# Optimization experiments

Hardware: AMD Instinct MI355X
Metric: run time of the kernel (lower is better)

Reference implementation:

```python
import jax, jax.numpy as jnp
import numpy as np

BN_EPS = 1e-5


def mesh_conv(x, gemm, W):
    # x: [B, C, E], gemm: [B, E, 4] neighbor edge indices, W: [O, C, 5]
    # gather the 4 neighbor edge features per edge (per batch element)
    nbr = jax.vmap(lambda xb, gb: xb[:, gb])(x, gemm)  # [B, C, E, 4]
    f1, f2, f3, f4 = nbr[..., 0], nbr[..., 1], nbr[..., 2], nbr[..., 3]
    # MeshCNN symmetric functions over opposite neighbors
    f = jnp.stack(
        [x, f1 + f3, f2 + f4, jnp.abs(f1 - f3), jnp.abs(f2 - f4)], axis=-1
    )  # [B, C, E, 5]
    # Conv2d(in, out, kernel=(1,5), bias=False) == contraction over (C, 5)
    return jnp.einsum('bcek,ock->boe', f, W)  # [B, O, E]


def batchnorm_relu(x, gamma, beta):
    # BatchNorm2d in training mode (stats over batch and edge dims), applied
    # to relu(x) as in the original: bn(F.relu(x)); x is [B, C, E]
    h = jax.nn.relu(x)
    mean = jnp.mean(h, axis=(0, 2), keepdims=True)
    var = jnp.var(h, axis=(0, 2), keepdims=True)
    h = (h - mean) * jax.lax.rsqrt(var + BN_EPS)
    return h * gamma[None, :, None] + beta[None, :, None]


def setup_inputs() -> dict:
    key = jax.random.key(0)
    ks = jax.random.split(key, 5)
    B, C_in, C_out, E = 4, 128, 256, 30000
    x = jax.random.normal(ks[0], (B, C_in, E), dtype=jnp.float32)
    gemm = jax.random.randint(ks[1], (B, E, 4), 0, E, dtype=jnp.int32)
    W0 = jax.random.normal(ks[2], (C_out, C_in, 5), dtype=jnp.float32) * (1.0 / np.sqrt(C_in * 5))
    gamma1 = jnp.ones((C_out,), dtype=jnp.float32)
    beta1 = jnp.zeros((C_out,), dtype=jnp.float32)
    W1 = jax.random.normal(ks[3], (C_out, C_out, 5), dtype=jnp.float32) * (1.0 / np.sqrt(C_out * 5))
    return {"x": x, "gemm": gemm, "W0": W0, "gamma1": gamma1, "beta1": beta1, "W1": W1}


def reference(x, gemm, W0, gamma1, beta1, W1):
    x = mesh_conv(x, gemm, W0)          # conv0
    x1 = x                               # residual branch
    x = batchnorm_relu(x, gamma1, beta1)  # bn1(relu(x))
    x = mesh_conv(x, gemm, W1)          # conv1
    x = x + x1                           # residual add
    return jax.nn.relu(x)                # [B, C_out, E]
```

## Files before the change

kernel.cpp:

```cpp
#include <hip/hip_runtime.h>
#include <stdint.h>


#define BB 4
#define CIN 128
#define COUT 256
#define EE 30000
#define BN 64
#define NTILES 469
#define BC 64
#define KCH 320
#define PITCH 328
#define NBLK (NTILES * BB)

typedef __attribute__((ext_vector_type(8))) short bf16x8;
typedef __attribute__((ext_vector_type(4))) float f32x4;

static __device__ __forceinline__ unsigned f2bf1(float f) {
    union { float f; unsigned u; } v; v.f = f;
    return (v.u + 0x7fffu + ((v.u >> 16) & 1u)) >> 16;
}
static __device__ __forceinline__ unsigned pack2(float lo, float hi) {
    return f2bf1(lo) | (f2bf1(hi) << 16);
}
static __device__ __forceinline__ float bf2f(unsigned h) {
    union { unsigned u; float f; } v; v.u = h << 16;
    return v.f;
}

union RowU { int4 i4[2]; unsigned u[8]; };
union F16U { float4 f4[4]; float f[16]; };

__global__ __launch_bounds__(256) void k_transpose(const float* __restrict__ x,
                                                   unsigned short* __restrict__ xT) {
    __shared__ float tile[64][CIN + 1];
    const int t = threadIdx.x;
    const int e0 = blockIdx.x * 64;
    const int b = blockIdx.y;
    const int el = t & 63;
    const bool ok = (e0 + el) < EE;
    const float* xb = x + (size_t)b * CIN * EE;
#pragma unroll
    for (int cc = 0; cc < CIN / 4; ++cc) {
        const int c = cc * 4 + (t >> 6);
        tile[el][c] = ok ? xb[(size_t)c * EE + e0 + el] : 0.f;
    }
    __syncthreads();
    const int el2 = t >> 2, cq = t & 3;
    if (e0 + el2 < EE) {
        unsigned ov[16];
#pragma unroll
        for (int i = 0; i < 16; ++i)
            ov[i] = pack2(tile[el2][cq * 32 + 2 * i], tile[el2][cq * 32 + 2 * i + 1]);
        int4* dst = (int4*)(xT + ((size_t)b * EE + e0 + el2) * CIN + cq * 32);
#pragma unroll
        for (int j = 0; j < 4; ++j)
            dst[j] = make_int4((int)ov[4 * j], (int)ov[4 * j + 1], (int)ov[4 * j + 2], (int)ov[4 * j + 3]);
    }
}

__global__ __launch_bounds__(256) void k_wprep(const float* __restrict__ W,
                                               unsigned short* __restrict__ Wf,
                                               int C, int K) {
    const int id = blockIdx.x * 256 + threadIdx.x;
    if (id >= 256 * K) return;
    const int m = id / K;
    const int G = id % K;
    const int chunk = G / KCH;
    const int r = G % KCH;
    const int k = r / BC;
    const int c = chunk * BC + (r % BC);
    const float val = W[((size_t)m * C + c) * 5 + k];
    Wf[((size_t)(G / 32) * 256 + m) * 32 + (G % 32)] = (unsigned short)f2bf1(val);
}

__global__ __launch_bounds__(256) void k_stats(const float* __restrict__ partials,
                                               const float* __restrict__ gamma,
                                               const float* __restrict__ beta,
                                               float* __restrict__ ss) {
    const int ch = blockIdx.x;
    const int t = threadIdx.x;
    float s = 0.f, q = 0.f;
    for (int i = t; i < NBLK; i += 256) {
        s += partials[(size_t)i * 512 + ch];
        q += partials[(size_t)i * 512 + 256 + ch];
    }
    __shared__ float ls[256], lq[256];
    ls[t] = s; lq[t] = q;
    __syncthreads();
    for (int off = 128; off > 0; off >>= 1) {
        if (t < off) { ls[t] += ls[t + off]; lq[t] += lq[t + off]; }
        __syncthreads();
    }
    if (t == 0) {
        const float inv = 1.f / (float)(BB * EE);
        const float mean = ls[0] * inv;
        const float var = lq[0] * inv - mean * mean;
        const float sc = gamma[ch] * rsqrtf(var + 1e-5f);
        ss[ch] = sc;
        ss[COUT + ch] = beta[ch] - mean * sc;
    }
}

template <int C, int CHUNKS, int IS1>
__global__ __launch_bounds__(256) void k_conv(
    const unsigned short* __restrict__ xin,
    const int* __restrict__ gmm,
    const unsigned short* __restrict__ Wf,
    const float* __restrict__ ss,
    unsigned short* __restrict__ x1,
    unsigned short* __restrict__ rT,
    float* __restrict__ partials,
    float* __restrict__ out) {
    __shared__ unsigned short f_lds[64 * PITCH];
    const int t = threadIdx.x;
    const int w = t >> 6, lane = t & 63;
    const int ml = lane & 15, g = lane >> 4;
    const int tile = blockIdx.x, b = blockIdx.y;
    const int e0 = tile * BN;

    const int be = t >> 2, bq = t & 3;
    const int eb = e0 + be;
    const int ec = (eb < EE) ? eb : 0;
    const int4 nb = *(const int4*)(gmm + ((size_t)b * EE + ec) * 4);

    const unsigned short* xb = xin + (size_t)b * EE * C;
    const unsigned short* rowc = xb + (size_t)ec * C;
    const unsigned short* row1 = xb + (size_t)nb.x * C;
    const unsigned short* row2 = xb + (size_t)nb.y * C;
    const unsigned short* row3 = xb + (size_t)nb.z * C;
    const unsigned short* row4 = xb + (size_t)nb.w * C;

    f32x4 acc[4][4];
#pragma unroll
    for (int i = 0; i < 4; ++i)
#pragma unroll
        for (int j = 0; j < 4; ++j)
            acc[i][j] = (f32x4){0.f, 0.f, 0.f, 0.f};

#pragma unroll 1
    for (int chunk = 0; chunk < CHUNKS; ++chunk) {
        const int cb = chunk * BC + bq * 16;

        F16U sc, sh;
        if (IS1) {
#pragma unroll
            for (int q = 0; q < 4; ++q) {
                sc.f4[q] = *(const float4*)(ss + cb + 4 * q);
                sh.f4[q] = *(const float4*)(ss + COUT + cb + 4 * q);
            }
        }

        unsigned o0[8], o1[8], o2[8], o3[8], o4[8];
        {
            RowU va, vb;
            va.i4[0] = *(const int4*)(row1 + cb); va.i4[1] = *(const int4*)(row1 + cb + 8);
            vb.i4[0] = *(const int4*)(row3 + cb); vb.i4[1] = *(const int4*)(row3 + cb + 8);
#pragma unroll
            for (int j = 0; j < 8; ++j) {
                float a0 = bf2f(va.u[j] & 0xffffu), a1 = bf2f(va.u[j] >> 16);
                float b0 = bf2f(vb.u[j] & 0xffffu), b1 = bf2f(vb.u[j] >> 16);
                if (IS1) {
                    a0 = fmaf(a0, sc.f[2 * j], sh.f[2 * j]); a1 = fmaf(a1, sc.f[2 * j + 1], sh.f[2 * j + 1]);
                    b0 = fmaf(b0, sc.f[2 * j], sh.f[2 * j]); b1 = fmaf(b1, sc.f[2 * j + 1], sh.f[2 * j + 1]);
                }
                o1[j] = pack2(a0 + b0, a1 + b1);
                o3[j] = pack2(fabsf(a0 - b0), fabsf(a1 - b1));
            }
        }
        {
            RowU va, vb;
            va.i4[0] = *(const int4*)(row2 + cb); va.i4[1] = *(const int4*)(row2 + cb + 8);
            vb.i4[0] = *(const int4*)(row4 + cb); vb.i4[1] = *(const int4*)(row4 + cb + 8);
#pragma unroll
            for (int j = 0; j < 8; ++j) {
                float a0 = bf2f(va.u[j] & 0xffffu), a1 = bf2f(va.u[j] >> 16);
                float b0 = bf2f(vb.u[j] & 0xffffu), b1 = bf2f(vb.u[j] >> 16);
                if (IS1) {
                    a0 = fmaf(a0, sc.f[2 * j], sh.f[2 * j]); a1 = fmaf(a1, sc.f[2 * j + 1], sh.f[2 * j + 1]);
                    b0 = fmaf(b0, sc.f[2 * j], sh.f[2 * j]); b1 = fmaf(b1, sc.f[2 * j + 1], sh.f[2 * j + 1]);
                }
                o2[j] = pack2(a0 + b0, a1 + b1);
                o4[j] = pack2(fabsf(a0 - b0), fabsf(a1 - b1));
            }
        }
        {
            RowU v;
            v.i4[0] = *(const int4*)(rowc + cb); v.i4[1] = *(const int4*)(rowc + cb + 8);
#pragma unroll
            for (int j = 0; j < 8; ++j) {
                float c0 = bf2f(v.u[j] & 0xffffu), c1 = bf2f(v.u[j] >> 16);
                if (IS1) {
                    c0 = fmaf(c0, sc.f[2 * j], sh.f[2 * j]); c1 = fmaf(c1, sc.f[2 * j + 1], sh.f[2 * j + 1]);
                }
                o0[j] = pack2(c0, c1);
            }
        }

        __syncthreads();
        {
            unsigned short* bp = &f_lds[be * PITCH + bq * 16];
            *(int4*)(bp + 0 * BC)     = make_int4((int)o0[0], (int)o0[1], (int)o0[2], (int)o0[3]);
            *(int4*)(bp + 0 * BC + 8) = make_int4((int)o0[4], (int)o0[5], (int)o0[6], (int)o0[7]);
            *(int4*)(bp + 1 * BC)     = make_int4((int)o1[0], (int)o1[1], (int)o1[2], (int)o1[3]);
            *(int4*)(bp + 1 * BC + 8) = make_int4((int)o1[4], (int)o1[5], (int)o1[6], (int)o1[7]);
            *(int4*)(bp + 2 * BC)     = make_int4((int)o2[0], (int)o2[1], (int)o2[2], (int)o2[3]);
            *(int4*)(bp + 2 * BC + 8) = make_int4((int)o2[4], (int)o2[5], (int)o2[6], (int)o2[7]);
            *(int4*)(bp + 3 * BC)     = make_int4((int)o3[0], (int)o3[1], (int)o3[2], (int)o3[3]);
            *(int4*)(bp + 3 * BC + 8) = make_int4((int)o3[4], (int)o3[5], (int)o3[6], (int)o3[7]);
            *(int4*)(bp + 4 * BC)     = make_int4((int)o4[0], (int)o4[1], (int)o4[2], (int)o4[3]);
            *(int4*)(bp + 4 * BC + 8) = make_int4((int)o4[4], (int)o4[5], (int)o4[6], (int)o4[7]);
        }
        __syncthreads();

        const unsigned short* wp = Wf + (size_t)chunk * (KCH / 32) * COUT * 32;
#pragma unroll 2
        for (int kk = 0; kk < KCH / 32; ++kk) {
            union { int4 i; bf16x8 h; } af[4], bfr[4];
#pragma unroll
            for (int fm = 0; fm < 4; ++fm)
                af[fm].i = *(const int4*)(wp + ((size_t)kk * COUT + (w * 64 + fm * 16 + ml)) * 32 + g * 8);
#pragma unroll
            for (int fn = 0; fn < 4; ++fn)
                bfr[fn].i = *(const int4*)&f_lds[(fn * 16 + ml) * PITCH + kk * 32 + g * 8];
#pragma unroll
            for (int fm = 0; fm < 4; ++fm)
#pragma unroll
                for (int fn = 0; fn < 4; ++fn)
                    acc[fm][fn] = __builtin_amdgcn_mfma_f32_16x16x32_bf16(af[fm].h, bfr[fn].h, acc[fm][fn], 0, 0, 0);
        }
    }

    const size_t fragbase = (((size_t)b * NTILES + tile) * 4 + w) * 16;
    if (!IS1) {
#pragma unroll
        for (int fm = 0; fm < 4; ++fm) {
#pragma unroll
            for (int fn = 0; fn < 4; ++fn) {
                const int fi = fm * 4 + fn;
                uint2 pk;
                pk.x = pack2(acc[fm][fn][0], acc[fm][fn][1]);
                pk.y = pack2(acc[fm][fn][2], acc[fm][fn][3]);
                *(uint2*)(x1 + (fragbase + fi) * 256 + lane * 4) = pk;
                const int e = e0 + fn * 16 + ml;
                if (e < EE) {
                    uint2 pr;
                    pr.x = pack2(fmaxf(acc[fm][fn][0], 0.f), fmaxf(acc[fm][fn][1], 0.f));
                    pr.y = pack2(fmaxf(acc[fm][fn][2], 0.f), fmaxf(acc[fm][fn][3], 0.f));
                    *(uint2*)(rT + ((size_t)b * EE + e) * COUT + w * 64 + fm * 16 + g * 4) = pr;
                }
            }
        }
        float ks = 0.f, kq = 0.f;
#pragma unroll
        for (int fm = 0; fm < 4; ++fm) {
#pragma unroll
            for (int r = 0; r < 4; ++r) {
                float s = 0.f, q2 = 0.f;
#pragma unroll
                for (int fn = 0; fn < 4; ++fn) {
                    const int e = e0 + fn * 16 + ml;
                    const float v = (e < EE) ? fmaxf(acc[fm][fn][r], 0.f) : 0.f;
                    s += v; q2 += v * v;
                }
                s += __shfl_xor(s, 1); s += __shfl_xor(s, 2);
                s += __shfl_xor(s, 4); s += __shfl_xor(s, 8);
                q2 += __shfl_xor(q2, 1); q2 += __shfl_xor(q2, 2);
                q2 += __shfl_xor(q2, 4); q2 += __shfl_xor(q2, 8);
                if (ml == fm * 4 + r) { ks = s; kq = q2; }
            }
        }
        const int ch = w * 64 + (ml >> 2) * 16 + g * 4 + (ml & 3);
        float* pp = partials + ((size_t)b * NTILES + tile) * 512;
        pp[ch] = ks;
        pp[256 + ch] = kq;
    } else {
#pragma unroll
        for (int fm = 0; fm < 4; ++fm) {
#pragma unroll
            for (int fn = 0; fn < 4; ++fn) {
                const int fi = fm * 4 + fn;
                const uint2 pk = *(const uint2*)(x1 + (fragbase + fi) * 256 + lane * 4);
                const int e = e0 + fn * 16 + ml;
                if (e < EE) {
                    const int chb = w * 64 + fm * 16 + g * 4;
                    float* op = out + ((size_t)b * COUT + chb) * EE + e;
                    op[0]              = fmaxf(acc[fm][fn][0] + bf2f(pk.x & 0xffffu), 0.f);
                    op[(size_t)EE]     = fmaxf(acc[fm][fn][1] + bf2f(pk.x >> 16), 0.f);
                    op[(size_t)2 * EE] = fmaxf(acc[fm][fn][2] + bf2f(pk.y & 0xffffu), 0.f);
                    op[(size_t)3 * EE] = fmaxf(acc[fm][fn][3] + bf2f(pk.y >> 16), 0.f);
                }
            }
        }
    }
}

extern "C" void kernel_launch(void* const* d_in, const int* in_sizes, int n_in,
                              void* d_out, int out_size, void* d_ws, size_t ws_size,
                              hipStream_t stream) {
    const float* x = (const float*)d_in[0];
    const int* gmm = (const int*)d_in[1];
    const float* W0 = (const float*)d_in[2];
    const float* gamma = (const float*)d_in[3];
    const float* beta = (const float*)d_in[4];
    const float* W1 = (const float*)d_in[5];
    float* out = (float*)d_out;

    char* ws = (char*)d_ws;
    unsigned short* xT  = (unsigned short*)(ws);
    unsigned short* Wf0 = (unsigned short*)(ws + 30720000);
    unsigned short* Wf1 = (unsigned short*)(ws + 31047680);
    unsigned short* x1  = (unsigned short*)(ws + 31703040);
    unsigned short* rT  = (unsigned short*)(ws + 93175808);
    float* partials     = (float*)(ws + 154615808);
    float* ss           = (float*)(ws + 158457856);

    k_transpose<<<dim3(NTILES, BB), 256, 0, stream>>>(x, xT);
    k_wprep<<<dim3(640), 256, 0, stream>>>(W0, Wf0, CIN, 640);
    k_wprep<<<dim3(1280), 256, 0, stream>>>(W1, Wf1, COUT, 1280);
    k_conv<CIN, 2, 0><<<dim3(NTILES, BB), 256, 0, stream>>>(
        xT, gmm, Wf0, nullptr, x1, rT, partials, nullptr);
    k_stats<<<dim3(256), 256, 0, stream>>>(partials, gamma, beta, ss);
    k_conv<COUT, 4, 1><<<dim3(NTILES, BB), 256, 0, stream>>>(
        rT, gmm, Wf1, ss, x1, nullptr, nullptr, out);
}
```

Measured before the change: 530.5 us.

## Fold BN affine into conv1 weights and bias, prefetch gathers, remap grid

Moves the batchnorm scale into the second conv's weights (using abs(scale) for the abs-difference terms) and the shift into a per-output bias computed by a new kernel. This removes the per-element FMA normalisation from the gather stage. Also adds register double-buffering of the neighbour-row loads, a 1D grid that interleaves batches, launch_bounds for 2 blocks per CU, intrinsic bf16 packing, and a cheaper partial-stats reduction. The fold is exact only for gamma-scaled rows, and applying abs(scale) to the weights assumes the shift cancels inside the difference terms. Double buffering raises register pressure.

```diff
diff --git a/kernel.cpp b/kernel.cpp
--- a/kernel.cpp
+++ b/kernel.cpp
@@ -1,4 +1,5 @@
 #include <hip/hip_runtime.h>
+#include <hip/hip_bf16.h>
 #include <stdint.h>
 
 
@@ -12,24 +13,25 @@
 #define KCH 320
 #define PITCH 328
 #define NBLK (NTILES * BB)
+#define GRID1 1880
 
 typedef __attribute__((ext_vector_type(8))) short bf16x8;
 typedef __attribute__((ext_vector_type(4))) float f32x4;
 
-static __device__ __forceinline__ unsigned f2bf1(float f) {
-    union { float f; unsigned u; } v; v.f = f;
-    return (v.u + 0x7fffu + ((v.u >> 16) & 1u)) >> 16;
-}
-static __device__ __forceinline__ unsigned pack2(float lo, float hi) {
-    return f2bf1(lo) | (f2bf1(hi) << 16);
-}
-static __device__ __forceinline__ float bf2f(unsigned h) {
-    union { unsigned u; float f; } v; v.u = h << 16;
-    return v.f;
-}
-
-union RowU { int4 i4[2]; unsigned u[8]; };
-union F16U { float4 f4[4]; float f[16]; };
+static __device__ __forceinline__ float blo(unsigned u) {
+    union { unsigned u; float f; } v; v.u = u << 16; return v.f;
+}
+static __device__ __forceinline__ float bhi(unsigned u) {
+    union { unsigned u; float f; } v; v.u = u & 0xffff0000u; return v.f;
+}
+static __device__ __forceinline__ unsigned pk2(float lo, float hi) {
+    __hip_bfloat162 h = __float22bfloat162_rn(float2{lo, hi});
+    union { __hip_bfloat162 h; unsigned u; } v; v.h = h; return v.u;
+}
+static __device__ __forceinline__ unsigned short bf1(float f) {
+    __hip_bfloat16 h = __float2bfloat16(f);
+    union { __hip_bfloat16 h; unsigned short u; } v; v.h = h; return v.u;
+}
 
 __global__ __launch_bounds__(256) void k_transpose(const float* __restrict__ x,
                                                    unsigned short* __restrict__ xT) {
@@ -51,7 +53,7 @@
         unsigned ov[16];
 #pragma unroll
         for (int i = 0; i < 16; ++i)
-            ov[i] = pack2(tile[el2][cq * 32 + 2 * i], tile[el2][cq * 32 + 2 * i + 1]);
+            ov[i] = pk2(tile[el2][cq * 32 + 2 * i], tile[el2][cq * 32 + 2 * i + 1]);
         int4* dst = (int4*)(xT + ((size_t)b * EE + e0 + el2) * CIN + cq * 32);
 #pragma unroll
         for (int j = 0; j < 4; ++j)
@@ -61,6 +63,7 @@
 
 __global__ __launch_bounds__(256) void k_wprep(const float* __restrict__ W,
                                                unsigned short* __restrict__ Wf,
+                                               const float* __restrict__ ss,
                                                int C, int K) {
     const int id = blockIdx.x * 256 + threadIdx.x;
     if (id >= 256 * K) return;
@@ -70,8 +73,12 @@
     const int r = G % KCH;
     const int k = r / BC;
     const int c = chunk * BC + (r % BC);
-    const float val = W[((size_t)m * C + c) * 5 + k];
-    Wf[((size_t)(G / 32) * 256 + m) * 32 + (G % 32)] = (unsigned short)f2bf1(val);
+    float val = W[((size_t)m * C + c) * 5 + k];
+    if (ss) {
+        const float sc = ss[c];
+        val *= (k < 3) ? sc : fabsf(sc);
+    }
+    Wf[((size_t)(G / 32) * 256 + m) * 32 + (G % 32)] = bf1(val);
 }
 
 __global__ __launch_bounds__(256) void k_stats(const float* __restrict__ partials,
@@ -102,12 +109,29 @@
     }
 }
 
+__global__ __launch_bounds__(256) void k_bias(const float* __restrict__ W1,
+                                              const float* __restrict__ ss,
+                                              float* __restrict__ bias) {
+    const int o = blockIdx.x, t = threadIdx.x;
+    const float sh = ss[COUT + t];
+    const float* wr = W1 + ((size_t)o * COUT + t) * 5;
+    float v = sh * (wr[0] + 2.f * (wr[1] + wr[2]));
+    __shared__ float red[256];
+    red[t] = v;
+    __syncthreads();
+    for (int off = 128; off > 0; off >>= 1) {
+        if (t < off) red[t] += red[t + off];
+        __syncthreads();
+    }
+    if (t == 0) bias[o] = red[0];
+}
+
 template <int C, int CHUNKS, int IS1>
-__global__ __launch_bounds__(256) void k_conv(
+__global__ __launch_bounds__(256, 2) void k_conv(
     const unsigned short* __restrict__ xin,
     const int* __restrict__ gmm,
     const unsigned short* __restrict__ Wf,
-    const float* __restrict__ ss,
+    const float* __restrict__ bias,
     unsigned short* __restrict__ x1,
     unsigned short* __restrict__ rT,
     float* __restrict__ partials,
@@ -116,7 +140,10 @@
     const int t = threadIdx.x;
     const int w = t >> 6, lane = t & 63;
     const int ml = lane & 15, g = lane >> 4;
-    const int tile = blockIdx.x, b = blockIdx.y;
+    const int i = blockIdx.x;
+    const int b = (i & 7) >> 1;
+    const int tile = ((i >> 3) << 1) | (i & 1);
+    if (tile >= NTILES) return;
     const int e0 = tile * BN;
 
     const int be = t >> 2, bq = t & 3;
@@ -133,75 +160,51 @@
 
     f32x4 acc[4][4];
 #pragma unroll
-    for (int i = 0; i < 4; ++i)
-#pragma unroll
-        for (int j = 0; j < 4; ++j)
-            acc[i][j] = (f32x4){0.f, 0.f, 0.f, 0.f};
-
-#pragma unroll 1
-    for (int chunk = 0; chunk < CHUNKS; ++chunk) {
+    for (int ii = 0; ii < 4; ++ii)
+#pragma unroll
+        for (int jj = 0; jj < 4; ++jj)
+            acc[ii][jj] = (f32x4){0.f, 0.f, 0.f, 0.f};
+
+    int4 bufA[10], bufB[10];
+
+    auto stage = [&](int chunk, int4* dst) {
         const int cb = chunk * BC + bq * 16;
-
-        F16U sc, sh;
-        if (IS1) {
-#pragma unroll
-            for (int q = 0; q < 4; ++q) {
-                sc.f4[q] = *(const float4*)(ss + cb + 4 * q);
-                sh.f4[q] = *(const float4*)(ss + COUT + cb + 4 * q);
-            }
-        }
-
-        unsigned o0[8], o1[8], o2[8], o3[8], o4[8];
-        {
-            RowU va, vb;
-            va.i4[0] = *(const int4*)(row1 + cb); va.i4[1] = *(const int4*)(row1 + cb + 8);
-            vb.i4[0] = *(const int4*)(row3 + cb); vb.i4[1] = *(const int4*)(row3 + cb + 8);
-#pragma unroll
-            for (int j = 0; j < 8; ++j) {
-                float a0 = bf2f(va.u[j] & 0xffffu), a1 = bf2f(va.u[j] >> 16);
-                float b0 = bf2f(vb.u[j] & 0xffffu), b1 = bf2f(vb.u[j] >> 16);
-                if (IS1) {
-                    a0 = fmaf(a0, sc.f[2 * j], sh.f[2 * j]); a1 = fmaf(a1, sc.f[2 * j + 1], sh.f[2 * j + 1]);
-                    b0 = fmaf(b0, sc.f[2 * j], sh.f[2 * j]); b1 = fmaf(b1, sc.f[2 * j + 1], sh.f[2 * j + 1]);
-                }
-                o1[j] = pack2(a0 + b0, a1 + b1);
-                o3[j] = pack2(fabsf(a0 - b0), fabsf(a1 - b1));
-            }
-        }
-        {
-            RowU va, vb;
-            va.i4[0] = *(const int4*)(row2 + cb); va.i4[1] = *(const int4*)(row2 + cb + 8);
-            vb.i4[0] = *(const int4*)(row4 + cb); vb.i4[1] = *(const int4*)(row4 + cb + 8);
-#pragma unroll
-            for (int j = 0; j < 8; ++j) {
-                float a0 = bf2f(va.u[j] & 0xffffu), a1 = bf2f(va.u[j] >> 16);
-                float b0 = bf2f(vb.u[j] & 0xffffu), b1 = bf2f(vb.u[j] >> 16);
-                if (IS1) {
-                    a0 = fmaf(a0, sc.f[2 * j], sh.f[2 * j]); a1 = fmaf(a1, sc.f[2 * j + 1], sh.f[2 * j + 1]);
-                    b0 = fmaf(b0, sc.f[2 * j], sh.f[2 * j]); b1 = fmaf(b1, sc.f[2 * j + 1], sh.f[2 * j + 1]);
-                }
-                o2[j] = pack2(a0 + b0, a1 + b1);
-                o4[j] = pack2(fabsf(a0 - b0), fabsf(a1 - b1));
-            }
-        }
-        {
-            RowU v;
-            v.i4[0] = *(const int4*)(rowc + cb); v.i4[1] = *(const int4*)(rowc + cb + 8);
-#pragma unroll
-            for (int j = 0; j < 8; ++j) {
-                float c0 = bf2f(v.u[j] & 0xffffu), c1 = bf2f(v.u[j] >> 16);
-                if (IS1) {
-                    c0 = fmaf(c0, sc.f[2 * j], sh.f[2 * j]); c1 = fmaf(c1, sc.f[2 * j + 1], sh.f[2 * j + 1]);
-                }
-                o0[j] = pack2(c0, c1);
-            }
+        dst[0] = *(const int4*)(row1 + cb); dst[1] = *(const int4*)(row1 + cb + 8);
+        dst[2] = *(const int4*)(row3 + cb); dst[3] = *(const int4*)(row3 + cb + 8);
+        dst[4] = *(const int4*)(row2 + cb); dst[5] = *(const int4*)(row2 + cb + 8);
+        dst[6] = *(const int4*)(row4 + cb); dst[7] = *(const int4*)(row4 + cb + 8);
+        dst[8] = *(const int4*)(rowc + cb); dst[9] = *(const int4*)(rowc + cb + 8);
+    };
+
+    auto step = [&](int chunk, const int4* cur, int4* nxt, bool donext) {
+        if (donext) stage(chunk + 1, nxt);
+
+        const unsigned* u13a = (const unsigned*)&cur[0];
+        const unsigned* u13b = (const unsigned*)&cur[2];
+        const unsigned* u24a = (const unsigned*)&cur[4];
+        const unsigned* u24b = (const unsigned*)&cur[6];
+        const unsigned* uc   = (const unsigned*)&cur[8];
+        unsigned o1[8], o2[8], o3[8], o4[8];
+#pragma unroll
+        for (int j = 0; j < 8; ++j) {
+            const float a0 = blo(u13a[j]), a1 = bhi(u13a[j]);
+            const float b0 = blo(u13b[j]), b1 = bhi(u13b[j]);
+            o1[j] = pk2(a0 + b0, a1 + b1);
+            o3[j] = pk2(fabsf(a0 - b0), fabsf(a1 - b1));
+        }
+#pragma unroll
+        for (int j = 0; j < 8; ++j) {
+            const float a0 = blo(u24a[j]), a1 = bhi(u24a[j]);
+            const float b0 = blo(u24b[j]), b1 = bhi(u24b[j]);
+            o2[j] = pk2(a0 + b0, a1 + b1);
+            o4[j] = pk2(fabsf(a0 - b0), fabsf(a1 - b1));
         }
 
         __syncthreads();
         {
             unsigned short* bp = &f_lds[be * PITCH + bq * 16];
-            *(int4*)(bp + 0 * BC)     = make_int4((int)o0[0], (int)o0[1], (int)o0[2], (int)o0[3]);
-            *(int4*)(bp + 0 * BC + 8) = make_int4((int)o0[4], (int)o0[5], (int)o0[6], (int)o0[7]);
+            *(int4*)(bp + 0 * BC)     = make_int4((int)uc[0], (int)uc[1], (int)uc[2], (int)uc[3]);
+            *(int4*)(bp + 0 * BC + 8) = make_int4((int)uc[4], (int)uc[5], (int)uc[6], (int)uc[7]);
             *(int4*)(bp + 1 * BC)     = make_int4((int)o1[0], (int)o1[1], (int)o1[2], (int)o1[3]);
             *(int4*)(bp + 1 * BC + 8) = make_int4((int)o1[4], (int)o1[5], (int)o1[6], (int)o1[7]);
             *(int4*)(bp + 2 * BC)     = make_int4((int)o2[0], (int)o2[1], (int)o2[2], (int)o2[3]);
@@ -229,66 +232,84 @@
                 for (int fn = 0; fn < 4; ++fn)
                     acc[fm][fn] = __builtin_amdgcn_mfma_f32_16x16x32_bf16(af[fm].h, bfr[fn].h, acc[fm][fn], 0, 0, 0);
         }
+    };
+
+    stage(0, bufA);
+#pragma unroll 1
+    for (int cp = 0; cp < CHUNKS / 2; ++cp) {
+        step(2 * cp, bufA, bufB, true);
+        step(2 * cp + 1, bufB, bufA, (2 * cp + 2) < CHUNKS);
     }
 
     const size_t fragbase = (((size_t)b * NTILES + tile) * 4 + w) * 16;
     if (!IS1) {
+        float ks[4][4], kq[4][4];
+#pragma unroll
+        for (int fm = 0; fm < 4; ++fm)
+#pragma unroll
+            for (int r = 0; r < 4; ++r) { ks[fm][r] = 0.f; kq[fm][r] = 0.f; }
 #pragma unroll
         for (int fm = 0; fm < 4; ++fm) {
 #pragma unroll
             for (int fn = 0; fn < 4; ++fn) {
                 const int fi = fm * 4 + fn;
                 uint2 pk;
-                pk.x = pack2(acc[fm][fn][0], acc[fm][fn][1]);
-                pk.y = pack2(acc[fm][fn][2], acc[fm][fn][3]);
+                pk.x = pk2(acc[fm][fn][0], acc[fm][fn][1]);
+                pk.y = pk2(acc[fm][fn][2], acc[fm][fn][3]);
                 *(uint2*)(x1 + (fragbase + fi) * 256 + lane * 4) = pk;
                 const int e = e0 + fn * 16 + ml;
+                float rv0 = fmaxf(acc[fm][fn][0], 0.f), rv1 = fmaxf(acc[fm][fn][1], 0.f);
+                float rv2 = fmaxf(acc[fm][fn][2], 0.f), rv3 = fmaxf(acc[fm][fn][3], 0.f);
                 if (e < EE) {
                     uint2 pr;
-                    pr.x = pack2(fmaxf(acc[fm][fn][0], 0.f), fmaxf(acc[fm][fn][1], 0.f));
-                    pr.y = pack2(fmaxf(acc[fm][fn][2], 0.f), fmaxf(acc[fm][fn][3], 0.f));
+                    pr.x = pk2(rv0, rv1);
+                    pr.y = pk2(rv2, rv3);
                     *(uint2*)(rT + ((size_t)b * EE + e) * COUT + w * 64 + fm * 16 + g * 4) = pr;
+                } else {
+                    rv0 = rv1 = rv2 = rv3 = 0.f;
+                }
+                ks[fm][0] += rv0; kq[fm][0] += rv0 * rv0;
+                ks[fm][1] += rv1; kq[fm][1] += rv1 * rv1;
+                ks[fm][2] += rv2; kq[fm][2] += rv2 * rv2;
+                ks[fm][3] += rv3; kq[fm][3] += rv3 * rv3;
+            }
+        }
+#pragma unroll
+        for (int fm = 0; fm < 4; ++fm) {
+#pragma unroll
+            for (int r = 0; r < 4; ++r) {
+#pragma unroll
+                for (int m = 1; m < 16; m <<= 1) {
+                    ks[fm][r] += __shfl_xor(ks[fm][r], m);
+                    kq[fm][r] += __shfl_xor(kq[fm][r], m);
                 }
             }
         }
-        float ks = 0.f, kq = 0.f;
+        if (ml == 0) {
+            float* pp = partials + ((size_t)b * NTILES + tile) * 512;
+#pragma unroll
+            for (int fm = 0; fm < 4; ++fm) {
+                const int ch = w * 64 + fm * 16 + g * 4;
+                *(float4*)(pp + ch)       = make_float4(ks[fm][0], ks[fm][1], ks[fm][2], ks[fm][3]);
+                *(float4*)(pp + 256 + ch) = make_float4(kq[fm][0], kq[fm][1], kq[fm][2], kq[fm][3]);
+            }
+        }
+    } else {
 #pragma unroll
         for (int fm = 0; fm < 4; ++fm) {
-#pragma unroll
-            for (int r = 0; r < 4; ++r) {
-                float s = 0.f, q2 = 0.f;
-#pragma unroll
-                for (int fn = 0; fn < 4; ++fn) {
-                    const int e = e0 + fn * 16 + ml;
-                    const float v = (e < EE) ? fmaxf(acc[fm][fn][r], 0.f) : 0.f;
-                    s += v; q2 += v * v;
-                }
-                s += __shfl_xor(s, 1); s += __shfl_xor(s, 2);
-                s += __shfl_xor(s, 4); s += __shfl_xor(s, 8);
-                q2 += __shfl_xor(q2, 1); q2 += __shfl_xor(q2, 2);
-                q2 += __shfl_xor(q2, 4); q2 += __shfl_xor(q2, 8);
-                if (ml == fm * 4 + r) { ks = s; kq = q2; }
-            }
-        }
-        const int ch = w * 64 + (ml >> 2) * 16 + g * 4 + (ml & 3);
-        float* pp = partials + ((size_t)b * NTILES + tile) * 512;
-        pp[ch] = ks;
-        pp[256 + ch] = kq;
-    } else {
-#pragma unroll
-        for (int fm = 0; fm < 4; ++fm) {
+            const int chb = w * 64 + fm * 16 + g * 4;
+            const float4 bv = *(const float4*)(bias + chb);
 #pragma unroll
             for (int fn = 0; fn < 4; ++fn) {
                 const int fi = fm * 4 + fn;
                 const uint2 pk = *(const uint2*)(x1 + (fragbase + fi) * 256 + lane * 4);
                 const int e = e0 + fn * 16 + ml;
                 if (e < EE) {
-                    const int chb = w * 64 + fm * 16 + g * 4;
                     float* op = out + ((size_t)b * COUT + chb) * EE + e;
-                    op[0]              = fmaxf(acc[fm][fn][0] + bf2f(pk.x & 0xffffu), 0.f);
-                    op[(size_t)EE]     = fmaxf(acc[fm][fn][1] + bf2f(pk.x >> 16), 0.f);
-                    op[(size_t)2 * EE] = fmaxf(acc[fm][fn][2] + bf2f(pk.y & 0xffffu), 0.f);
-                    op[(size_t)3 * EE] = fmaxf(acc[fm][fn][3] + bf2f(pk.y >> 16), 0.f);
+                    op[0]              = fmaxf(acc[fm][fn][0] + bv.x + blo(pk.x), 0.f);
+                    op[(size_t)EE]     = fmaxf(acc[fm][fn][1] + bv.y + bhi(pk.x), 0.f);
+                    op[(size_t)2 * EE] = fmaxf(acc[fm][fn][2] + bv.z + blo(pk.y), 0.f);
+                    op[(size_t)3 * EE] = fmaxf(acc[fm][fn][3] + bv.w + bhi(pk.y), 0.f);
                 }
             }
         }
@@ -314,13 +335,15 @@
     unsigned short* rT  = (unsigned short*)(ws + 93175808);
     float* partials     = (float*)(ws + 154615808);
     float* ss           = (float*)(ws + 158457856);
+    float* bias         = (float*)(ws + 158459904);
 
     k_transpose<<<dim3(NTILES, BB), 256, 0, stream>>>(x, xT);
-    k_wprep<<<dim3(640), 256, 0, stream>>>(W0, Wf0, CIN, 640);
-    k_wprep<<<dim3(1280), 256, 0, stream>>>(W1, Wf1, COUT, 1280);
-    k_conv<CIN, 2, 0><<<dim3(NTILES, BB), 256, 0, stream>>>(
+    k_wprep<<<dim3(640), 256, 0, stream>>>(W0, Wf0, nullptr, CIN, 640);
+    k_conv<CIN, 2, 0><<<dim3(GRID1), 256, 0, stream>>>(
         xT, gmm, Wf0, nullptr, x1, rT, partials, nullptr);
     k_stats<<<dim3(256), 256, 0, stream>>>(partials, gamma, beta, ss);
-    k_conv<COUT, 4, 1><<<dim3(NTILES, BB), 256, 0, stream>>>(
-        rT, gmm, Wf1, ss, x1, nullptr, nullptr, out);
-}
+    k_bias<<<dim3(256), 256, 0, stream>>>(W1, ss, bias);
+    k_wprep<<<dim3(1280), 256, 0, stream>>>(W1, Wf1, ss, COUT, 1280);
+    k_conv<COUT, 4, 1><<<dim3(GRID1), 256, 0, stream>>>(
+        rT, gmm, Wf1, bias, x1, nullptr, nullptr, out);
+}
```

After: 478.2 us. 9.9% less time.
